# Kernel optimization log

Hardware: AMD Instinct MI355X
Metric: run time of the kernel (lower is better)

Reference implementation:

```python
import jax, jax.numpy as jnp
import numpy as np

Q, C, T, D_IN, D_H = 512, 512, 128, 512, 256


def setup_inputs() -> dict:
    key = jax.random.key(0)
    ks = jax.random.split(key, 8)
    s_in = 1.0 / np.sqrt(D_IN)
    s_h = 1.0 / np.sqrt(D_H)
    return {
        "audio": jax.random.normal(ks[0], (Q, T, D_IN), jnp.float32),
        "video": jax.random.normal(ks[1], (C, T, D_IN), jnp.float32),
        "a_w1": jax.random.normal(ks[2], (D_IN, D_H), jnp.float32) * s_in,
        "a_b1": jnp.zeros((D_H,), jnp.float32),
        "a_w2": jax.random.normal(ks[3], (D_H, D_H), jnp.float32) * s_h,
        "a_b2": jnp.zeros((D_H,), jnp.float32),
        "v_w1": jax.random.normal(ks[4], (D_IN, D_H), jnp.float32) * s_in,
        "v_b1": jnp.zeros((D_H,), jnp.float32),
        "v_w2": jax.random.normal(ks[5], (D_H, D_H), jnp.float32) * s_h,
        "v_b2": jnp.zeros((D_H,), jnp.float32),
        "W": jax.random.normal(ks[6], (D_H, D_H), jnp.float32) * s_h,
        "max_lag": 4,
    }


def _mlp(x, w1, b1, w2, b2):
    # Linear -> ReLU -> Linear
    h = jnp.maximum(x @ w1 + b1, 0.0)
    return h @ w2 + b2


def reference(audio, video, a_w1, a_b1, a_w2, a_b2,
              v_w1, v_b1, v_w2, v_b2, W, max_lag):
    a = _mlp(audio, a_w1, a_b1, a_w2, a_b2)   # [Q, T, D_H]
    v = _mlp(video, v_w1, v_b1, v_w2, v_b2)   # [C, T, D_H]
    # roll along time commutes with the per-frame linear map, so project once
    pv = jnp.einsum('ctd,df->ctf', v, W)      # [C, T, D_H]
    best = None
    for delta in range(-max_lag, max_lag + 1):
        shifted = jnp.roll(pv, delta, axis=1)
        score = jnp.einsum('qtd,ctd->qc', a, shifted)  # [Q, C]
        best = score if best is None else jnp.maximum(best, score)
    return best
```

## Files before the change

kernel.cpp:

```cpp
#include <hip/hip_runtime.h>
#include <cstdint>
#include <cstddef>

typedef __attribute__((ext_vector_type(8))) short frag8;
typedef __attribute__((ext_vector_type(4))) float f32x4;

static __device__ __forceinline__ unsigned short f2bf_r(float f) {
    return (unsigned short)((__float_as_uint(f) + 0x8000u) >> 16);
}

static __device__ __forceinline__ void gll16(const void* g, void* l) {
    __builtin_amdgcn_global_load_lds(
        (const __attribute__((address_space(1))) unsigned int*)g,
        (__attribute__((address_space(3))) unsigned int*)l, 16, 0, 0);
}

__global__ __launch_bounds__(256, 2)
void mlp_fused(const float* __restrict__ X0, const float* __restrict__ X1,
               const unsigned short* __restrict__ W1T0, const unsigned short* __restrict__ W1T1,
               const float* __restrict__ b1v0, const float* __restrict__ b1v1,
               const unsigned short* __restrict__ W2T0, const unsigned short* __restrict__ W2T1,
               const float* __restrict__ b2v0, const float* __restrict__ b2v1,
               unsigned short* __restrict__ O0, unsigned short* __restrict__ O1)
{
    __shared__ __align__(16) unsigned short As[64 * 72];
    __shared__ __align__(16) unsigned short Bs[256 * 64];
    __shared__ __align__(16) unsigned short hs[64 * 264];

    const int mod = blockIdx.y;
    const float* X = mod ? X1 : X0;
    const unsigned short* W1T = mod ? W1T1 : W1T0;
    const unsigned short* W2T = mod ? W2T1 : W2T0;
    const float* b1 = mod ? b1v1 : b1v0;
    const float* b2 = mod ? b2v1 : b2v0;
    unsigned short* O = mod ? O1 : O0;

    const int t    = threadIdx.x;
    const int wave = t >> 6;
    const int lane = t & 63;
    const int quad = lane >> 4;
    const int l15  = lane & 15;
    const int m0   = blockIdx.x * 64;

    const int rowB = lane >> 3;
    const int qB   = (lane & 7) ^ rowB;
    const int nRowBase = wave * 64 + rowB;
    unsigned short* BsW = Bs + wave * 4096;
    const int swz = l15 & 7;

    f32x4 acc[4][4];
    #pragma unroll
    for (int i = 0; i < 4; ++i)
        #pragma unroll
        for (int j = 0; j < 4; ++j)
            acc[i][j] = (f32x4){0.f, 0.f, 0.f, 0.f};

    for (int k0 = 0; k0 < 512; k0 += 64) {
        #pragma unroll
        for (int p = 0; p < 4; ++p) {
            const int idx = p * 256 + t;
            const int row = idx >> 4;
            const int col = (idx & 15) * 4;
            const float4 v = *(const float4*)(X + (size_t)(m0 + row) * 512 + k0 + col);
            const unsigned int a0 = __float_as_uint(v.x) + 0x8000u;
            const unsigned int a1 = __float_as_uint(v.y) + 0x8000u;
            const unsigned int a2 = __float_as_uint(v.z) + 0x8000u;
            const unsigned int a3 = __float_as_uint(v.w) + 0x8000u;
            uint2 pk;
            pk.x = __builtin_amdgcn_perm(a1, a0, 0x07060302u);
            pk.y = __builtin_amdgcn_perm(a3, a2, 0x07060302u);
            *(uint2*)&As[row * 72 + col] = pk;
        }
        #pragma unroll
        for (int p = 0; p < 8; ++p)
            gll16(W1T + (size_t)(nRowBase + p * 8) * 512 + qB * 8 + k0, BsW + p * 512);
        __syncthreads();

        frag8 af[2][4], bf[2][4];
        #pragma unroll
        for (int i = 0; i < 4; ++i)
            #pragma unroll
            for (int kh = 0; kh < 2; ++kh)
                af[kh][i] = *(const frag8*)&As[(i * 16 + l15) * 72 + kh * 32 + quad * 8];
        #pragma unroll
        for (int j = 0; j < 4; ++j) {
            const int row = wave * 64 + j * 16 + l15;
            #pragma unroll
            for (int kh = 0; kh < 2; ++kh)
                bf[kh][j] = *(const frag8*)&Bs[row * 64 + (((kh * 4 + quad) ^ swz) * 8)];
        }
        #pragma unroll
        for (int kh = 0; kh < 2; ++kh)
            #pragma unroll
            for (int i = 0; i < 4; ++i)
                #pragma unroll
                for (int j = 0; j < 4; ++j)
                    acc[i][j] = __builtin_amdgcn_mfma_f32_16x16x32_bf16(af[kh][i], bf[kh][j], acc[i][j], 0, 0, 0);
        __syncthreads();
    }

    #pragma unroll
    for (int j = 0; j < 4; ++j) {
        const int col = wave * 64 + j * 16 + l15;
        const float bv = b1[col];
        #pragma unroll
        for (int i = 0; i < 4; ++i) {
            const int rl = i * 16 + quad * 4;
            #pragma unroll
            for (int r = 0; r < 4; ++r)
                hs[(rl + r) * 264 + col] = f2bf_r(fmaxf(acc[i][j][r] + bv, 0.0f));
        }
    }
    __syncthreads();

    #pragma unroll
    for (int i = 0; i < 4; ++i)
        #pragma unroll
        for (int j = 0; j < 4; ++j)
            acc[i][j] = (f32x4){0.f, 0.f, 0.f, 0.f};

    for (int k0 = 0; k0 < 256; k0 += 64) {
        #pragma unroll
        for (int p = 0; p < 8; ++p)
            gll16(W2T + (size_t)(nRowBase + p * 8) * 256 + qB * 8 + k0, BsW + p * 512);
        __syncthreads();

        frag8 af[2][4], bf[2][4];
        #pragma unroll
        for (int i = 0; i < 4; ++i)
            #pragma unroll
            for (int kh = 0; kh < 2; ++kh)
                af[kh][i] = *(const frag8*)&hs[(i * 16 + l15) * 264 + k0 + kh * 32 + quad * 8];
        #pragma unroll
        for (int j = 0; j < 4; ++j) {
            const int row = wave * 64 + j * 16 + l15;
            #pragma unroll
            for (int kh = 0; kh < 2; ++kh)
                bf[kh][j] = *(const frag8*)&Bs[row * 64 + (((kh * 4 + quad) ^ swz) * 8)];
        }
        #pragma unroll
        for (int kh = 0; kh < 2; ++kh)
            #pragma unroll
            for (int i = 0; i < 4; ++i)
                #pragma unroll
                for (int j = 0; j < 4; ++j)
                    acc[i][j] = __builtin_amdgcn_mfma_f32_16x16x32_bf16(af[kh][i], bf[kh][j], acc[i][j], 0, 0, 0);
        __syncthreads();
    }

    #pragma unroll
    for (int j = 0; j < 4; ++j) {
        const int col = wave * 64 + j * 16 + l15;
        const float bv = b2[col];
        #pragma unroll
        for (int i = 0; i < 4; ++i) {
            const int rl = i * 16 + quad * 4;
            #pragma unroll
            for (int r = 0; r < 4; ++r)
                hs[(rl + r) * 264 + col] = f2bf_r(acc[i][j][r] + bv);
        }
    }
    __syncthreads();
    #pragma unroll
    for (int u = 0; u < 8; ++u) {
        const int chunk = u * 256 + t;
        const int row = chunk >> 5;
        const int c16 = (chunk & 31) * 8;
        uint4 v = *(const uint4*)&hs[row * 264 + c16];
        *(uint4*)&O[(size_t)(m0 + row) * 256 + c16] = v;
    }
}

__global__ __launch_bounds__(512, 2)
void gemm_corr(const unsigned short* __restrict__ A, const unsigned short* __restrict__ B,
               float* __restrict__ partial, int sc)
{
    __shared__ __align__(16) unsigned short lds[4][2][8192];

    const int t    = threadIdx.x;
    const int wave = t >> 6;
    const int lane = t & 63;
    const int quad = lane >> 4;
    const int l15  = lane & 15;
    const int wr   = wave >> 2;
    const int wc   = wave & 3;
    const int m0   = blockIdx.y * 256;
    const int n0   = blockIdx.x * 256;

    const int z = blockIdx.z;
    int d, s, t0, nT;
    if (sc == 7) { d = z / 7; s = z - d * 7; nT = (s == 6) ? 136 : 148; t0 = s * 148; }
    else         { d = z >> 2; s = z & 3;    nT = 256;                  t0 = s << 8; }
    const int delta  = d - 4;
    const int kStart = t0 * 32;
    const int koff   = (32768 - 256 * delta) & 32767;

    const int gsrc      = (lane & 7) ^ ((lane >> 3) & 7);
    const int srcRowOff = ((lane >> 3) << 1) + (gsrc >> 2);
    const int srcCol    = (gsrc & 3) << 3;
    const size_t aSrcBase = (size_t)(m0 + srcRowOff) * 32768 + srcCol;
    const size_t bSrcBase = (size_t)(n0 + srcRowOff) * 32768 + srcCol;

    const int gphys = (((l15 & 1) << 2) | quad) ^ ((l15 >> 1) & 7);
    const int aOff  = (wr * 64 + (l15 >> 1)) * 64 + gphys * 8;
    const int bOff  = (wc * 32 + (l15 >> 1)) * 64 + gphys * 8;

    f32x4 acc[8][4];
    #pragma unroll
    for (int i = 0; i < 8; ++i)
        #pragma unroll
        for (int j = 0; j < 4; ++j)
            acc[i][j] = (f32x4){0.f, 0.f, 0.f, 0.f};

    #pragma unroll
    for (int pt = 0; pt < 3; ++pt) {
        const int kk = (kStart + pt * 32) & 32767;
        const int kb = (kk + koff) & 32767;
        #pragma unroll
        for (int qq = 0; qq < 2; ++qq) {
            const int c = wave * 2 + qq;
            gll16(A + aSrcBase + (size_t)c * 16 * 32768 + kk, &lds[pt][0][c * 512]);
            gll16(B + bSrcBase + (size_t)c * 16 * 32768 + kb, &lds[pt][1][c * 512]);
        }
    }

    for (int kt0 = 0; kt0 < nT; kt0 += 4) {
        #pragma unroll
        for (int u = 0; u < 4; ++u) {
            {
                const int kk = (kStart + (kt0 + u + 3) * 32) & 32767;
                const int kb = (kk + koff) & 32767;
                unsigned short* LSa = &lds[(u + 3) & 3][0][wave * 1024];
                unsigned short* LSb = &lds[(u + 3) & 3][1][wave * 1024];
                #pragma unroll
                for (int qq = 0; qq < 2; ++qq) {
                    const int c = wave * 2 + qq;
                    gll16(A + aSrcBase + (size_t)c * 16 * 32768 + kk, LSa + qq * 512);
                    gll16(B + bSrcBase + (size_t)c * 16 * 32768 + kb, LSb + qq * 512);
                }
            }
            asm volatile("s_waitcnt vmcnt(12)" ::: "memory");
            __builtin_amdgcn_s_barrier();
            asm volatile("" ::: "memory");

            const unsigned short* LA = lds[u][0];
            const unsigned short* LB = lds[u][1];
            frag8 af[8], bf[4];
            #pragma unroll
            for (int j = 0; j < 4; ++j) bf[j] = *(const frag8*)(LB + bOff + j * 512);
            #pragma unroll
            for (int i = 0; i < 4; ++i) af[i] = *(const frag8*)(LA + aOff + i * 512);
            __builtin_amdgcn_s_setprio(1);
            #pragma unroll
            for (int i = 0; i < 4; ++i)
                #pragma unroll
                for (int j = 0; j < 4; ++j)
                    acc[i][j] = __builtin_amdgcn_mfma_f32_16x16x32_bf16(af[i], bf[j], acc[i][j], 0, 0, 0);
            __builtin_amdgcn_s_setprio(0);
            #pragma unroll
            for (int i = 4; i < 8; ++i) af[i] = *(const frag8*)(LA + aOff + i * 512);
            __builtin_amdgcn_s_setprio(1);
            #pragma unroll
            for (int i = 4; i < 8; ++i)
                #pragma unroll
                for (int j = 0; j < 4; ++j)
                    acc[i][j] = __builtin_amdgcn_mfma_f32_16x16x32_bf16(af[i], bf[j], acc[i][j], 0, 0, 0);
            __builtin_amdgcn_s_setprio(0);
            asm volatile("" ::: "memory");
            __builtin_amdgcn_s_barrier();
        }
    }
    asm volatile("s_waitcnt vmcnt(0)" ::: "memory");

    float* C = partial + ((size_t)z << 18);
    #pragma unroll
    for (int i = 0; i < 8; ++i) {
        const int rg = m0 + wr * 128 + i * 16 + quad * 4;
        #pragma unroll
        for (int j = 0; j < 4; ++j) {
            const int cg = n0 + wc * 64 + j * 16 + l15;
            #pragma unroll
            for (int r = 0; r < 4; ++r)
                C[(size_t)(rg + r) * 512 + cg] = acc[i][j][r];
        }
    }
}

__global__ void prep(const float* __restrict__ a_w1, const float* __restrict__ v_w1,
                     const float* __restrict__ a_w2, const float* __restrict__ v_w2,
                     const float* __restrict__ W, const float* __restrict__ v_b2,
                     unsigned short* __restrict__ aw1T, unsigned short* __restrict__ vw1T,
                     unsigned short* __restrict__ aw2T,
                     unsigned short* __restrict__ WcT, float* __restrict__ bc)
{
    const int b = blockIdx.x;
    __shared__ float tl[32][33];
    __shared__ float wcol[256];
    if (b < 320) {
        const float* src; unsigned short* dst; int R, C, tile;
        if (b < 128)      { src = a_w1; dst = aw1T; R = 512; C = 256; tile = b; }
        else if (b < 256) { src = v_w1; dst = vw1T; R = 512; C = 256; tile = b - 128; }
        else              { src = a_w2; dst = aw2T; R = 256; C = 256; tile = b - 256; }
        const int tilesX = C / 32;
        const int bx = (tile % tilesX) * 32, by = (tile / tilesX) * 32;
        const int tx = threadIdx.x & 31, ty = threadIdx.x >> 5;
        #pragma unroll
        for (int r = ty; r < 32; r += 8)
            tl[r][tx] = src[(size_t)(by + r) * C + bx + tx];
        __syncthreads();
        #pragma unroll
        for (int c = ty; c < 32; c += 8)
            dst[(size_t)(bx + c) * R + by + tx] = f2bf_r(tl[tx][c]);
    } else {
        const int n = b - 320, k = threadIdx.x;
        wcol[k] = W[(size_t)k * 256 + n];
        __syncthreads();
        float s = 0.f;
        #pragma unroll 8
        for (int d = 0; d < 256; ++d) s += v_w2[(size_t)k * 256 + d] * wcol[d];
        WcT[(size_t)n * 256 + k] = f2bf_r(s);
        if (k == 0) {
            float tt = 0.f;
            for (int d = 0; d < 256; ++d) tt += v_b2[d] * wcol[d];
            bc[n] = tt;
        }
    }
}

__global__ void reduce_max(const float* __restrict__ partial, float* __restrict__ out, int sc) {
    const int idx = blockIdx.x * blockDim.x + threadIdx.x;
    float best = -3.4e38f;
    for (int d = 0; d < 9; ++d) {
        float ssum = 0.f;
        const float* p = partial + ((size_t)(d * sc) << 18) + idx;
        for (int k = 0; k < sc; ++k) ssum += p[(size_t)k << 18];
        best = fmaxf(best, ssum);
    }
    out[idx] = best;
}

extern "C" void kernel_launch(void* const* d_in, const int* in_sizes, int n_in,
                              void* d_out, int out_size, void* d_ws, size_t ws_size,
                              hipStream_t stream) {
    const float* audio = (const float*)d_in[0];
    const float* video = (const float*)d_in[1];
    const float* a_w1  = (const float*)d_in[2];
    const float* a_b1  = (const float*)d_in[3];
    const float* a_w2  = (const float*)d_in[4];
    const float* a_b2  = (const float*)d_in[5];
    const float* v_w1  = (const float*)d_in[6];
    const float* v_b1  = (const float*)d_in[7];
    const float* v_w2  = (const float*)d_in[8];
    const float* v_b2  = (const float*)d_in[9];
    const float* Wm    = (const float*)d_in[10];

    char* ws = (char*)d_ws;
    unsigned short* aw1T = (unsigned short*)(ws + 0);
    unsigned short* vw1T = (unsigned short*)(ws + 262144);
    unsigned short* aw2T = (unsigned short*)(ws + 524288);
    unsigned short* WcT  = (unsigned short*)(ws + 655360);
    float*          bc   = (float*)(ws + 786432);
    unsigned short* a_bf = (unsigned short*)(ws + 1048576);
    unsigned short* pv   = (unsigned short*)(ws + 34603008);
    float* partial       = (float*)(ws + 68157440);
    float* out = (float*)d_out;

    const int sc = (ws_size >= 134217728ull) ? 7 : 4;

    prep<<<dim3(576), 256, 0, stream>>>(a_w1, v_w1, a_w2, v_w2, Wm, v_b2,
                                        aw1T, vw1T, aw2T, WcT, bc);
    mlp_fused<<<dim3(1024, 2), 256, 0, stream>>>(
        audio, video, aw1T, vw1T, a_b1, v_b1, aw2T, WcT, a_b2, bc, a_bf, pv);
    gemm_corr<<<dim3(2, 2, 9 * sc), 512, 0, stream>>>(a_bf, pv, partial, sc);
    reduce_max<<<dim3(1024), 256, 0, stream>>>(partial, out, sc);
}
```

Measured before the change: 489.6 us.

## Remap gemm_corr blocks across XCDs and prefetch MLP input registers

In gemm_corr the launch-order block index is remapped so that consecutive logical tiles (same lag and K-slice, neighbouring M/N tiles) land on the same XCD, which should improve per-XCD L2 reuse of the A and B panels. The partial-output index is recomputed from the remapped coordinates. In mlp_fused the next K-chunk of X is loaded into registers before the MFMA loop, so global latency is hidden behind compute, and the MFMA sections get raised wave priority. The cost is more register pressure in mlp_fused and a mapping that assumes particular grid sizes.

```diff
diff --git a/kernel.cpp b/kernel.cpp
--- a/kernel.cpp
+++ b/kernel.cpp
@@ -48,6 +48,9 @@
     unsigned short* BsW = Bs + wave * 4096;
     const int swz = l15 & 7;
 
+    const int sRow = t >> 4;
+    const int sCol = (t & 15) * 4;
+
     f32x4 acc[4][4];
     #pragma unroll
     for (int i = 0; i < 4; ++i)
@@ -55,13 +58,15 @@
         for (int j = 0; j < 4; ++j)
             acc[i][j] = (f32x4){0.f, 0.f, 0.f, 0.f};
 
+    float4 xr[4];
+    #pragma unroll
+    for (int p = 0; p < 4; ++p)
+        xr[p] = *(const float4*)(X + (size_t)(m0 + p * 16 + sRow) * 512 + sCol);
+
     for (int k0 = 0; k0 < 512; k0 += 64) {
         #pragma unroll
         for (int p = 0; p < 4; ++p) {
-            const int idx = p * 256 + t;
-            const int row = idx >> 4;
-            const int col = (idx & 15) * 4;
-            const float4 v = *(const float4*)(X + (size_t)(m0 + row) * 512 + k0 + col);
+            const float4 v = xr[p];
             const unsigned int a0 = __float_as_uint(v.x) + 0x8000u;
             const unsigned int a1 = __float_as_uint(v.y) + 0x8000u;
             const unsigned int a2 = __float_as_uint(v.z) + 0x8000u;
@@ -69,13 +74,19 @@
             uint2 pk;
             pk.x = __builtin_amdgcn_perm(a1, a0, 0x07060302u);
             pk.y = __builtin_amdgcn_perm(a3, a2, 0x07060302u);
-            *(uint2*)&As[row * 72 + col] = pk;
+            *(uint2*)&As[(p * 16 + sRow) * 72 + sCol] = pk;
         }
         #pragma unroll
         for (int p = 0; p < 8; ++p)
             gll16(W1T + (size_t)(nRowBase + p * 8) * 512 + qB * 8 + k0, BsW + p * 512);
         __syncthreads();
 
+        if (k0 + 64 < 512) {
+            #pragma unroll
+            for (int p = 0; p < 4; ++p)
+                xr[p] = *(const float4*)(X + (size_t)(m0 + p * 16 + sRow) * 512 + (k0 + 64) + sCol);
+        }
+
         frag8 af[2][4], bf[2][4];
         #pragma unroll
         for (int i = 0; i < 4; ++i)
@@ -89,6 +100,7 @@
             for (int kh = 0; kh < 2; ++kh)
                 bf[kh][j] = *(const frag8*)&Bs[row * 64 + (((kh * 4 + quad) ^ swz) * 8)];
         }
+        __builtin_amdgcn_s_setprio(1);
         #pragma unroll
         for (int kh = 0; kh < 2; ++kh)
             #pragma unroll
@@ -96,6 +108,7 @@
                 #pragma unroll
                 for (int j = 0; j < 4; ++j)
                     acc[i][j] = __builtin_amdgcn_mfma_f32_16x16x32_bf16(af[kh][i], bf[kh][j], acc[i][j], 0, 0, 0);
+        __builtin_amdgcn_s_setprio(0);
         __syncthreads();
     }
 
@@ -138,6 +151,7 @@
             for (int kh = 0; kh < 2; ++kh)
                 bf[kh][j] = *(const frag8*)&Bs[row * 64 + (((kh * 4 + quad) ^ swz) * 8)];
         }
+        __builtin_amdgcn_s_setprio(1);
         #pragma unroll
         for (int kh = 0; kh < 2; ++kh)
             #pragma unroll
@@ -145,6 +159,7 @@
                 #pragma unroll
                 for (int j = 0; j < 4; ++j)
                     acc[i][j] = __builtin_amdgcn_mfma_f32_16x16x32_bf16(af[kh][i], bf[kh][j], acc[i][j], 0, 0, 0);
+        __builtin_amdgcn_s_setprio(0);
         __syncthreads();
     }
 
@@ -175,7 +190,7 @@
 void gemm_corr(const unsigned short* __restrict__ A, const unsigned short* __restrict__ B,
                float* __restrict__ partial, int sc)
 {
-    __shared__ __align__(16) unsigned short lds[4][2][8192];
+    __shared__ __align__(16) unsigned short lds[4 * 2 * 8192];
 
     const int t    = threadIdx.x;
     const int wave = t >> 6;
@@ -184,13 +199,28 @@
     const int l15  = lane & 15;
     const int wr   = wave >> 2;
     const int wc   = wave & 3;
-    const int m0   = blockIdx.y * 256;
-    const int n0   = blockIdx.x * 256;
-
-    const int z = blockIdx.z;
-    int d, s, t0, nT;
-    if (sc == 7) { d = z / 7; s = z - d * 7; nT = (s == 6) ? 136 : 148; t0 = s * 148; }
-    else         { d = z >> 2; s = z & 3;    nT = 256;                  t0 = s << 8; }
+
+    const int L = blockIdx.x + (blockIdx.y << 1) + (blockIdx.z << 2);
+    int ell;
+    if (sc == 7) {
+        const int xcd = L & 7, off = L >> 3;
+        ell = (xcd < 4 ? xcd * 32 : 128 + (xcd - 4) * 31) + off;
+    } else {
+        const int xcd = L & 7, off = L >> 3;
+        ell = xcd * 18 + off;
+    }
+    const int bx   = ell & 1;
+    const int by   = (ell >> 1) & 1;
+    const int rest = ell >> 2;
+    const int d    = rest % 9;
+    const int s    = rest / 9;
+    const int m0   = by * 256;
+    const int n0   = bx * 256;
+
+    int t0, nT;
+    if (sc == 7) { nT = (s == 6) ? 136 : 148; t0 = s * 148; }
+    else         { nT = 256;                  t0 = s << 8; }
+    const int zp     = d * sc + s;
     const int delta  = d - 4;
     const int kStart = t0 * 32;
     const int koff   = (32768 - 256 * delta) & 32767;
@@ -219,8 +249,8 @@
         #pragma unroll
         for (int qq = 0; qq < 2; ++qq) {
             const int c = wave * 2 + qq;
-            gll16(A + aSrcBase + (size_t)c * 16 * 32768 + kk, &lds[pt][0][c * 512]);
-            gll16(B + bSrcBase + (size_t)c * 16 * 32768 + kb, &lds[pt][1][c * 512]);
+            gll16(A + aSrcBase + (size_t)c * 16 * 32768 + kk, &lds[pt * 16384 + c * 512]);
+            gll16(B + bSrcBase + (size_t)c * 16 * 32768 + kb, &lds[pt * 16384 + 8192 + c * 512]);
         }
     }
 
@@ -230,8 +260,8 @@
             {
                 const int kk = (kStart + (kt0 + u + 3) * 32) & 32767;
                 const int kb = (kk + koff) & 32767;
-                unsigned short* LSa = &lds[(u + 3) & 3][0][wave * 1024];
-                unsigned short* LSb = &lds[(u + 3) & 3][1][wave * 1024];
+                unsigned short* LSa = &lds[((u + 3) & 3) * 16384 + wave * 1024];
+                unsigned short* LSb = LSa + 8192;
                 #pragma unroll
                 for (int qq = 0; qq < 2; ++qq) {
                     const int c = wave * 2 + qq;
@@ -243,8 +273,8 @@
             __builtin_amdgcn_s_barrier();
             asm volatile("" ::: "memory");
 
-            const unsigned short* LA = lds[u][0];
-            const unsigned short* LB = lds[u][1];
+            const unsigned short* LA = &lds[u * 16384];
+            const unsigned short* LB = LA + 8192;
             frag8 af[8], bf[4];
             #pragma unroll
             for (int j = 0; j < 4; ++j) bf[j] = *(const frag8*)(LB + bOff + j * 512);
@@ -272,7 +302,7 @@
     }
     asm volatile("s_waitcnt vmcnt(0)" ::: "memory");
 
-    float* C = partial + ((size_t)z << 18);
+    float* C = partial + ((size_t)zp << 18);
     #pragma unroll
     for (int i = 0; i < 8; ++i) {
         const int rg = m0 + wr * 128 + i * 16 + quad * 4;
```

Measured after the change: 513.3 us. 4.8% more time.
